# Optimization experiments

Measured on AMD Instinct MI355X. Metric: run time of the kernel, lower is better.

The kernel has to match this reference:

```python
import jax, jax.numpy as jnp
import numpy as np

ALG = 8  # octonion algebra dimension
_TRIPLES = [(1,2,3),(1,4,5),(1,7,6),(2,4,6),(2,5,7),(3,4,7),(3,6,5)]

def _oct_table():
    # Cayley multiplication table: e_i * e_j = S[i,j] * e_{K[i,j]}
    K = np.zeros((8,8), np.int64); S = np.zeros((8,8), np.int64)
    K[0,:] = np.arange(8); S[0,:] = 1
    K[:,0] = np.arange(8); S[:,0] = 1
    for i in range(1,8):
        K[i,i] = 0; S[i,i] = -1
    for (a,b,c) in _TRIPLES:
        for x,y,z in ((a,b,c),(b,c,a),(c,a,b)):
            K[x,y] = z; S[x,y] = 1
            K[y,x] = z; S[y,x] = -1
    return K, S

_K, _S = _oct_table()

def _ternary(w):
    # BitNet-style absmean ternary quantization (STE is irrelevant for fwd)
    scale = jnp.mean(jnp.abs(w)) + 1e-8
    wq = jnp.clip(jnp.round(w / scale), -1.0, 1.0) * scale
    return w + jax.lax.stop_gradient(wq - w)

def _oct_big(w):
    # w: [8, din8, dout8] -> structured dense [8*din8, 8*dout8]
    # out_k = sum_{i,j: e_i e_j = s e_k} s * x_i @ W_j  (64 static blocks)
    din8, dout8 = w.shape[1], w.shape[2]
    big = jnp.zeros((8, din8, 8, dout8), w.dtype)
    for i in range(8):
        for j in range(8):
            big = big.at[i, :, int(_K[i, j]), :].set(float(_S[i, j]) * w[j])
    return big.reshape(8 * din8, 8 * dout8)

def _oct_linear(x, w):
    return x @ _oct_big(_ternary(w))

def setup_inputs() -> dict:
    key = jax.random.key(0)
    k1, k2, k3, k4 = jax.random.split(key, 4)
    B, T, D = 8, 4096, 768
    H = 2048  # int(2*4*768/3) rounded up to multiple of 8
    d8, h8 = D // ALG, H // ALG
    x = jax.random.normal(k1, (B, T, D), dtype=jnp.float32)
    w_gate = 0.02 * jax.random.normal(k2, (ALG, d8, h8), dtype=jnp.float32)
    w_up   = 0.02 * jax.random.normal(k3, (ALG, d8, h8), dtype=jnp.float32)
    w_down = 0.02 * jax.random.normal(k4, (ALG, h8, d8), dtype=jnp.float32)
    return {"x": x, "w_gate": w_gate, "w_up": w_up, "w_down": w_down}

def reference(x, w_gate, w_up, w_down):
    gate = _oct_linear(x, w_gate)          # [B,T,H]
    up   = _oct_linear(x, w_up)            # [B,T,H]
    h    = jax.nn.silu(gate) * up          # SwiGLU gate
    return _oct_linear(h, w_down)          # [B,T,D]
```

## Files before the change

### kernel.cpp

```cpp
#include <hip/hip_runtime.h>
#include <hip/hip_bf16.h>

typedef unsigned short u16;
typedef unsigned int u32;
typedef float f32x4 __attribute__((ext_vector_type(4)));
typedef __bf16 bf16x8 __attribute__((ext_vector_type(8)));

#define AS1 __attribute__((address_space(1)))
#define AS3 __attribute__((address_space(3)))

#define MTOT 32768
#define DK   768
#define HN   2048

__constant__ signed char J_TAB[64] = {
  0,1,2,3,4,5,6,7,
  1,0,3,2,5,4,7,6,
  2,3,0,1,6,7,4,5,
  3,2,1,0,7,6,5,4,
  4,5,6,7,0,1,2,3,
  5,4,7,6,1,0,3,2,
  6,7,4,5,2,3,0,1,
  7,6,5,4,3,2,1,0};
__constant__ signed char S_TAB[64] = {
   1, 1, 1, 1, 1, 1, 1, 1,
  -1, 1,-1, 1,-1, 1, 1,-1,
  -1, 1, 1,-1,-1,-1, 1, 1,
  -1,-1, 1, 1,-1, 1,-1, 1,
  -1, 1, 1, 1, 1,-1,-1,-1,
  -1,-1, 1,-1, 1, 1, 1,-1,
  -1,-1,-1, 1, 1,-1, 1, 1,
  -1, 1,-1,-1, 1, 1,-1, 1};

__device__ __forceinline__ u16 f2bf(float f) {
  u32 x = __float_as_uint(f);
  x += 0x7fffu + ((x >> 16) & 1u);
  return (u16)(x >> 16);
}

__device__ __forceinline__ void gload_lds16(const void* g, void* l) {
  __builtin_amdgcn_global_load_lds((AS1 void*)(g), (AS3 void*)(l), 16, 0, 0);
}

#define VMW(N) do { __builtin_amdgcn_sched_barrier(0); \
  asm volatile("s_waitcnt vmcnt(" #N ")" ::: "memory"); \
  __builtin_amdgcn_sched_barrier(0); } while (0)
#define BAR() do { __builtin_amdgcn_sched_barrier(0); \
  __builtin_amdgcn_s_barrier(); \
  __builtin_amdgcn_sched_barrier(0); } while (0)

template <int LDK>
__device__ __forceinline__ void stage_half(const u16* __restrict__ src,
                                           u16* lds, int tid) {
#pragma unroll
  for (int f0 = 0; f0 < 1024; f0 += 512) {
    int flat = f0 + tid;
    int row = flat >> 3;
    int c = (flat & 7) ^ (row & 7);
    gload_lds16(src + row * LDK + c * 8, lds + (f0 + (tid & ~63)) * 8);
  }
}

template <int LDK, bool SA, bool SB, int VM>
__device__ __forceinline__ void ktile4(
    const u16* lAp, const u16* lBp, u16* lAn, u16* lBn,
    const u16* __restrict__ aStage, const u16* __restrict__ bStage,
    int tid, int arow, int brow, int c0, int c1, f32x4 (&acc)[8][4]) {
  bf16x8 a0[4], a1[4], a2[4], a3[4], b0[4], b1[4];
#pragma unroll
  for (int mi = 0; mi < 4; ++mi)
    a0[mi] = *(const bf16x8*)(lAp + (arow + mi * 16) * 64 + c0);
#pragma unroll
  for (int ni = 0; ni < 4; ++ni)
    b0[ni] = *(const bf16x8*)(lBp + (brow + ni * 16) * 64 + c0);
#pragma unroll
  for (int mi = 0; mi < 4; ++mi)
    a1[mi] = *(const bf16x8*)(lAp + (arow + mi * 16) * 64 + c1);
#pragma unroll
  for (int ni = 0; ni < 4; ++ni)
    b1[ni] = *(const bf16x8*)(lBp + (brow + ni * 16) * 64 + c1);
  if constexpr (SA) stage_half<LDK>(aStage, lAn, tid);
  BAR();
  __builtin_amdgcn_s_setprio(1);
#pragma unroll
  for (int mi = 0; mi < 4; ++mi)
#pragma unroll
    for (int ni = 0; ni < 4; ++ni)
      acc[mi][ni] = __builtin_amdgcn_mfma_f32_16x16x32_bf16(
          a0[mi], b0[ni], acc[mi][ni], 0, 0, 0);
  __builtin_amdgcn_s_setprio(0);
  BAR();
#pragma unroll
  for (int mi = 0; mi < 4; ++mi)
    a2[mi] = *(const bf16x8*)(lAp + (arow + 64 + mi * 16) * 64 + c0);
  if constexpr (SA) stage_half<LDK>(aStage + 128 * LDK, lAn + 128 * 64, tid);
  BAR();
  __builtin_amdgcn_s_setprio(1);
#pragma unroll
  for (int mi = 0; mi < 4; ++mi)
#pragma unroll
    for (int ni = 0; ni < 4; ++ni)
      acc[mi][ni] = __builtin_amdgcn_mfma_f32_16x16x32_bf16(
          a1[mi], b1[ni], acc[mi][ni], 0, 0, 0);
  __builtin_amdgcn_s_setprio(0);
  BAR();
#pragma unroll
  for (int mi = 0; mi < 4; ++mi)
    a3[mi] = *(const bf16x8*)(lAp + (arow + 64 + mi * 16) * 64 + c1);
  if constexpr (SB) stage_half<LDK>(bStage, lBn, tid);
  BAR();
  __builtin_amdgcn_s_setprio(1);
#pragma unroll
  for (int mi = 0; mi < 4; ++mi)
#pragma unroll
    for (int ni = 0; ni < 4; ++ni)
      acc[4 + mi][ni] = __builtin_amdgcn_mfma_f32_16x16x32_bf16(
          a2[mi], b0[ni], acc[4 + mi][ni], 0, 0, 0);
  __builtin_amdgcn_s_setprio(0);
  BAR();
  if constexpr (SB) stage_half<LDK>(bStage + 128 * LDK, lBn + 128 * 64, tid);
  if constexpr (VM == 4) VMW(4);
  else if constexpr (VM == 0) VMW(0);
  BAR();
  __builtin_amdgcn_s_setprio(1);
#pragma unroll
  for (int mi = 0; mi < 4; ++mi)
#pragma unroll
    for (int ni = 0; ni < 4; ++ni)
      acc[4 + mi][ni] = __builtin_amdgcn_mfma_f32_16x16x32_bf16(
          a3[mi], b1[ni], acc[4 + mi][ni], 0, 0, 0);
  __builtin_amdgcn_s_setprio(0);
  BAR();
}

template <int NK, int LDK>
__device__ __forceinline__ void gemm_core(const u16* __restrict__ aSrc,
                                          const u16* __restrict__ bSrc, int tid,
                                          u16* lA0, u16* lA1, u16* lB0, u16* lB1,
                                          f32x4 (&acc)[8][4]) {
  const int lane = tid & 63;
  const int wave = tid >> 6;
  const int wm = wave >> 2, wn = wave & 3;
  const int l15 = lane & 15, quad = (lane >> 4) & 3;
  const int arow = wm * 128 + l15;
  const int brow = wn * 64 + l15;
  const int c0 = (quad ^ (l15 & 7)) * 8;
  const int c1 = ((quad + 4) ^ (l15 & 7)) * 8;

  stage_half<LDK>(aSrc, lA0, tid);
  stage_half<LDK>(aSrc + 128 * LDK, lA0 + 128 * 64, tid);
  stage_half<LDK>(bSrc, lB0, tid);
  stage_half<LDK>(bSrc + 128 * LDK, lB0 + 128 * 64, tid);
  stage_half<LDK>(bSrc + 64, lB1, tid);
  stage_half<LDK>(bSrc + 64 + 128 * LDK, lB1 + 128 * 64, tid);
  VMW(4);
  BAR();

#pragma unroll 1
  for (int i = 0; i < NK / 2 - 1; ++i) {
    ktile4<LDK, true, true, 4>(lA0, lB0, lA1, lB0,
                               aSrc + (2 * i + 1) * 64, bSrc + (2 * i + 2) * 64,
                               tid, arow, brow, c0, c1, acc);
    ktile4<LDK, true, true, 4>(lA1, lB1, lA0, lB1,
                               aSrc + (2 * i + 2) * 64, bSrc + (2 * i + 3) * 64,
                               tid, arow, brow, c0, c1, acc);
  }
  ktile4<LDK, true, false, 0>(lA0, lB0, lA1, lB0,
                              aSrc + (NK - 1) * 64, nullptr,
                              tid, arow, brow, c0, c1, acc);
  ktile4<LDK, false, false, -1>(lA1, lB1, lA0, lB1, nullptr, nullptr,
                                tid, arow, brow, c0, c1, acc);
}

template <bool ST, int VM>
__device__ __forceinline__ void ktile2(
    const u16* lAp, const u16* lBp, u16* lAs, u16* lBs,
    const u16* __restrict__ aS, const u16* __restrict__ bS,
    int tid, int arow, int brow, int c0, int c1, f32x4 (&acc)[4][4]) {
  bf16x8 a0[4], a1[4], b0[4], b1[4];
#pragma unroll
  for (int mi = 0; mi < 4; ++mi)
    a0[mi] = *(const bf16x8*)(lAp + (arow + mi * 16) * 64 + c0);
#pragma unroll
  for (int ni = 0; ni < 4; ++ni)
    b0[ni] = *(const bf16x8*)(lBp + (brow + ni * 16) * 64 + c0);
#pragma unroll
  for (int mi = 0; mi < 4; ++mi)
    a1[mi] = *(const bf16x8*)(lAp + (arow + mi * 16) * 64 + c1);
#pragma unroll
  for (int ni = 0; ni < 4; ++ni)
    b1[ni] = *(const bf16x8*)(lBp + (brow + ni * 16) * 64 + c1);
  if constexpr (ST) stage_half<HN>(aS, lAs, tid);
  BAR();
  __builtin_amdgcn_s_setprio(1);
#pragma unroll
  for (int mi = 0; mi < 4; ++mi)
#pragma unroll
    for (int ni = 0; ni < 4; ++ni)
      acc[mi][ni] = __builtin_amdgcn_mfma_f32_16x16x32_bf16(
          a0[mi], b0[ni], acc[mi][ni], 0, 0, 0);
  __builtin_amdgcn_s_setprio(0);
  BAR();
  if constexpr (ST) {
    stage_half<HN>(bS, lBs, tid);
    stage_half<HN>(bS + 128 * HN, lBs + 128 * 64, tid);
  }
  if constexpr (VM == 6) VMW(6);
  else if constexpr (VM == 0) VMW(0);
  BAR();
  __builtin_amdgcn_s_setprio(1);
#pragma unroll
  for (int mi = 0; mi < 4; ++mi)
#pragma unroll
    for (int ni = 0; ni < 4; ++ni)
      acc[mi][ni] = __builtin_amdgcn_mfma_f32_16x16x32_bf16(
          a1[mi], b1[ni], acc[mi][ni], 0, 0, 0);
  __builtin_amdgcn_s_setprio(0);
  BAR();
}

__global__ void scales1_kernel(const float* __restrict__ w0,
                               const float* __restrict__ w1,
                               const float* __restrict__ w2,
                               float* __restrict__ partials) {
  __shared__ float red[256];
  const int t = blockIdx.x / 192;
  const int chunk = blockIdx.x % 192;
  const float* w = (t == 0) ? w0 : (t == 1) ? w1 : w2;
  const float4* w4 = (const float4*)(w + chunk * 1024);
  float4 v = w4[threadIdx.x];
  red[threadIdx.x] = fabsf(v.x) + fabsf(v.y) + fabsf(v.z) + fabsf(v.w);
  __syncthreads();
  for (int off = 128; off; off >>= 1) {
    if (threadIdx.x < off) red[threadIdx.x] += red[threadIdx.x + off];
    __syncthreads();
  }
  if (threadIdx.x == 0) partials[blockIdx.x] = red[0];
}

__global__ void scales2_kernel(const float* __restrict__ partials,
                               float* __restrict__ scales) {
  __shared__ float red[256];
  float s = (threadIdx.x < 192) ? partials[blockIdx.x * 192 + threadIdx.x] : 0.f;
  red[threadIdx.x] = s;
  __syncthreads();
  for (int off = 128; off; off >>= 1) {
    if (threadIdx.x < off) red[threadIdx.x] += red[threadIdx.x + off];
    __syncthreads();
  }
  if (threadIdx.x == 0) scales[blockIdx.x] = red[0] / 196608.f + 1e-8f;
}

__global__ void build_big_kernel(const float* __restrict__ w,
                                 const float* __restrict__ scales, int sidx,
                                 int A, int B, int ilv, u16* __restrict__ dst) {
  int idx = blockIdx.x * 256 + threadIdx.x;
  int K8 = 8 * A;
  int n = idx / K8;
  int k = idx - n * K8;
  int i = k / A, a = k - i * A;
  int c = n / B, b = n - c * B;
  float scale = scales[sidx];
  int j = J_TAB[i * 8 + c];
  float q = rintf(w[(j * A + a) * B + b] / scale);
  q = fminf(1.f, fmaxf(-1.f, q));
  int nd = (ilv >= 0) ? (((n & ~15) << 1) | (ilv << 4) | (n & 15)) : n;
  int kd = (ilv == -2) ? ((k & ~31) | ((k & 15) << 1) | ((k >> 4) & 1)) : k;
  dst[nd * K8 + kd] = f2bf(q * (float)S_TAB[i * 8 + c]);
}

__global__ void cvt_x_kernel(const float* __restrict__ x, u16* __restrict__ xb) {
  int gid = blockIdx.x * 256 + threadIdx.x;
  const float4* x4 = (const float4*)x;
  float4 v0 = x4[gid * 2], v1 = x4[gid * 2 + 1];
  uint4 o;
  o.x = (u32)f2bf(v0.x) | ((u32)f2bf(v0.y) << 16);
  o.y = (u32)f2bf(v0.z) | ((u32)f2bf(v0.w) << 16);
  o.z = (u32)f2bf(v1.x) | ((u32)f2bf(v1.y) << 16);
  o.w = (u32)f2bf(v1.z) | ((u32)f2bf(v1.w) << 16);
  ((uint4*)xb)[gid] = o;
}

__global__ __launch_bounds__(512, 2) void gemm1_kernel(
    const u16* __restrict__ xb, const u16* __restrict__ wgu,
    const float* __restrict__ scales, u16* __restrict__ h) {
  __shared__ __align__(16) u16 lA0[256 * 64], lA1[256 * 64];
  __shared__ __align__(16) u16 lB0[256 * 64], lB1[256 * 64];
  const int tid = threadIdx.x;
  const int logical = (blockIdx.x & 7) * 256 + (blockIdx.x >> 3);
  const int bn = logical & 15;
  const int bm = logical >> 4;
  const int m0 = bm * 256, n0 = bn * 256;

  f32x4 acc[8][4] = {};
  gemm_core<12, DK>(xb + (size_t)m0 * DK, wgu + (size_t)n0 * DK, tid,
                    lA0, lA1, lB0, lB1, acc);

  const int lane = tid & 63, wave = tid >> 6;
  const int wm = wave >> 2, wn = wave & 3;
  const int l15 = lane & 15, quad = lane >> 4;
  const float sg = scales[0], su = scales[1];
  const int a_ = bn * 4 + wn;
  u32* h32 = (u32*)h;
#pragma unroll
  for (int mi = 0; mi < 8; ++mi)
#pragma unroll
    for (int r = 0; r < 4; ++r) {
      int m = m0 + wm * 128 + mi * 16 + quad * 4 + r;
      float g0 = acc[mi][0][r] * sg, u0 = acc[mi][1][r] * su;
      float g1 = acc[mi][2][r] * sg, u1 = acc[mi][3][r] * su;
      float h0 = g0 / (1.f + __expf(-g0)) * u0;
      float h1 = g1 / (1.f + __expf(-g1)) * u1;
      h32[(size_t)m * (HN / 2) + a_ * 16 + l15] =
          (u32)f2bf(h0) | ((u32)f2bf(h1) << 16);
    }
}

__global__ __launch_bounds__(512, 2) void gemm2_kernel(
    const u16* __restrict__ h, const u16* __restrict__ wd,
    const float* __restrict__ scales, float* __restrict__ out) {
  __shared__ __align__(16) u16 lA[3][128 * 64];
  __shared__ __align__(16) u16 lB[3][256 * 64];
  const int tid = threadIdx.x;
  const int logical = (blockIdx.x & 7) * 96 + (blockIdx.x >> 3);
  const int bn = logical % 3;
  const int bm = logical / 3;
  const int m0 = bm * 128, n0 = bn * 256;
  const u16* aSrc = h + (size_t)m0 * HN;
  const u16* bSrc = wd + (size_t)n0 * HN;

  const int lane = tid & 63, wave = tid >> 6;
  const int wm = wave >> 2, wn = wave & 3;
  const int l15 = lane & 15, quad = (lane >> 4) & 3;
  const int arow = wm * 64 + l15;
  const int brow = wn * 64 + l15;
  const int c0 = (quad ^ (l15 & 7)) * 8;
  const int c1 = ((quad + 4) ^ (l15 & 7)) * 8;

  f32x4 acc[4][4] = {};

  stage_half<HN>(aSrc, lA[0], tid);
  stage_half<HN>(bSrc, lB[0], tid);
  stage_half<HN>(bSrc + 128 * HN, lB[0] + 128 * 64, tid);
  stage_half<HN>(aSrc + 64, lA[1], tid);
  stage_half<HN>(bSrc + 64, lB[1], tid);
  stage_half<HN>(bSrc + 64 + 128 * HN, lB[1] + 128 * 64, tid);
  VMW(6);
  BAR();

  u16 *pA0 = lA[0], *pA1 = lA[1], *pA2 = lA[2];
  u16 *pB0 = lB[0], *pB1 = lB[1], *pB2 = lB[2];
#pragma unroll 1
  for (int S = 0; S < (HN / 64) - 2; ++S) {
    ktile2<true, 6>(pA0, pB0, pA2, pB2,
                    aSrc + (S + 2) * 64, bSrc + (S + 2) * 64,
                    tid, arow, brow, c0, c1, acc);
    u16* tA = pA0; pA0 = pA1; pA1 = pA2; pA2 = tA;
    u16* tB = pB0; pB0 = pB1; pB1 = pB2; pB2 = tB;
  }
  ktile2<false, 0>(pA0, pB0, nullptr, nullptr, nullptr, nullptr,
                   tid, arow, brow, c0, c1, acc);
  ktile2<false, -1>(pA1, pB1, nullptr, nullptr, nullptr, nullptr,
                    tid, arow, brow, c0, c1, acc);

  const float sd = scales[2];
#pragma unroll
  for (int mi = 0; mi < 4; ++mi)
#pragma unroll
    for (int ni = 0; ni < 4; ++ni) {
      const int n = n0 + wn * 64 + ni * 16 + l15;
#pragma unroll
      for (int r = 0; r < 4; ++r) {
        int m = m0 + wm * 64 + mi * 16 + quad * 4 + r;
        out[(size_t)m * DK + n] = acc[mi][ni][r] * sd;
      }
    }
}

extern "C" void kernel_launch(void* const* d_in, const int* in_sizes, int n_in,
                              void* d_out, int out_size, void* d_ws, size_t ws_size,
                              hipStream_t stream) {
  const float* x      = (const float*)d_in[0];
  const float* w_gate = (const float*)d_in[1];
  const float* w_up   = (const float*)d_in[2];
  const float* w_down = (const float*)d_in[3];
  float* out = (float*)d_out;

  char* ws = (char*)d_ws;
  float* scales   = (float*)ws;
  float* partials = (float*)(ws + 256);
  u16* wgu = (u16*)(ws + 4096);
  u16* wd  = (u16*)(ws + 4096 + 6291456u);
  u16* xb  = (u16*)(ws + 4096 + 9437184u);
  u16* h   = (u16*)(ws + 4096 + 9437184u + 50331648u);

  scales1_kernel<<<576, 256, 0, stream>>>(w_gate, w_up, w_down, partials);
  scales2_kernel<<<3, 256, 0, stream>>>(partials, scales);
  build_big_kernel<<<6144, 256, 0, stream>>>(w_gate, scales, 0, 96, 256, 0, wgu);
  build_big_kernel<<<6144, 256, 0, stream>>>(w_up,   scales, 1, 96, 256, 1, wgu);
  build_big_kernel<<<6144, 256, 0, stream>>>(w_down, scales, 2, 256, 96, -2, wd);
  cvt_x_kernel<<<12288, 256, 0, stream>>>(x, xb);
  gemm1_kernel<<<2048, 512, 0, stream>>>(xb, wgu, scales, h);
  gemm2_kernel<<<768, 512, 0, stream>>>(h, wd, scales, out);
}
```

Before: 552.1 us.

## Shrink gemm2 tile to 64x256 with 4 waves and double buffering

Rewrites the down-projection GEMM to use 256-thread blocks, each computing a 64x256 output tile, with a simple two-stage LDS double buffer in place of the three-stage split-half pipeline. The launch grows to 1536 blocks, which gives more blocks per CU and spreads work more evenly across the device. The cost is lower arithmetic intensity per block: the 256-row B tile is reloaded for half as many A rows, raising global and LDS traffic. The simpler schedule also does less to overlap loads with MFMA work.

```diff
diff --git a/kernel.cpp b/kernel.cpp
--- a/kernel.cpp
+++ b/kernel.cpp
@@ -61,6 +61,18 @@
   }
 }
 
+template <int ROWS, int LDK>
+__device__ __forceinline__ void stage_tile(const u16* __restrict__ src,
+                                           u16* lds, int tid) {
+#pragma unroll
+  for (int f0 = 0; f0 < ROWS * 8; f0 += 256) {
+    int flat = f0 + tid;
+    int row = flat >> 3;
+    int c = (flat & 7) ^ (row & 7);
+    gload_lds16(src + row * LDK + c * 8, lds + (f0 + (tid & 192)) * 8);
+  }
+}
+
 template <int LDK, bool SA, bool SB, int VM>
 __device__ __forceinline__ void ktile4(
     const u16* lAp, const u16* lBp, u16* lAn, u16* lBn,
@@ -170,53 +182,6 @@
                               tid, arow, brow, c0, c1, acc);
   ktile4<LDK, false, false, -1>(lA1, lB1, lA0, lB1, nullptr, nullptr,
                                 tid, arow, brow, c0, c1, acc);
-}
-
-template <bool ST, int VM>
-__device__ __forceinline__ void ktile2(
-    const u16* lAp, const u16* lBp, u16* lAs, u16* lBs,
-    const u16* __restrict__ aS, const u16* __restrict__ bS,
-    int tid, int arow, int brow, int c0, int c1, f32x4 (&acc)[4][4]) {
-  bf16x8 a0[4], a1[4], b0[4], b1[4];
-#pragma unroll
-  for (int mi = 0; mi < 4; ++mi)
-    a0[mi] = *(const bf16x8*)(lAp + (arow + mi * 16) * 64 + c0);
-#pragma unroll
-  for (int ni = 0; ni < 4; ++ni)
-    b0[ni] = *(const bf16x8*)(lBp + (brow + ni * 16) * 64 + c0);
-#pragma unroll
-  for (int mi = 0; mi < 4; ++mi)
-    a1[mi] = *(const bf16x8*)(lAp + (arow + mi * 16) * 64 + c1);
-#pragma unroll
-  for (int ni = 0; ni < 4; ++ni)
-    b1[ni] = *(const bf16x8*)(lBp + (brow + ni * 16) * 64 + c1);
-  if constexpr (ST) stage_half<HN>(aS, lAs, tid);
-  BAR();
-  __builtin_amdgcn_s_setprio(1);
-#pragma unroll
-  for (int mi = 0; mi < 4; ++mi)
-#pragma unroll
-    for (int ni = 0; ni < 4; ++ni)
-      acc[mi][ni] = __builtin_amdgcn_mfma_f32_16x16x32_bf16(
-          a0[mi], b0[ni], acc[mi][ni], 0, 0, 0);
-  __builtin_amdgcn_s_setprio(0);
-  BAR();
-  if constexpr (ST) {
-    stage_half<HN>(bS, lBs, tid);
-    stage_half<HN>(bS + 128 * HN, lBs + 128 * 64, tid);
-  }
-  if constexpr (VM == 6) VMW(6);
-  else if constexpr (VM == 0) VMW(0);
-  BAR();
-  __builtin_amdgcn_s_setprio(1);
-#pragma unroll
-  for (int mi = 0; mi < 4; ++mi)
-#pragma unroll
-    for (int ni = 0; ni < 4; ++ni)
-      acc[mi][ni] = __builtin_amdgcn_mfma_f32_16x16x32_bf16(
-          a1[mi], b1[ni], acc[mi][ni], 0, 0, 0);
-  __builtin_amdgcn_s_setprio(0);
-  BAR();
 }
 
 __global__ void scales1_kernel(const float* __restrict__ w0,
@@ -316,62 +281,77 @@
     }
 }
 
-__global__ __launch_bounds__(512, 2) void gemm2_kernel(
+__global__ __launch_bounds__(256, 2) void gemm2_kernel(
     const u16* __restrict__ h, const u16* __restrict__ wd,
     const float* __restrict__ scales, float* __restrict__ out) {
-  __shared__ __align__(16) u16 lA[3][128 * 64];
-  __shared__ __align__(16) u16 lB[3][256 * 64];
+  __shared__ __align__(16) u16 lA[2][64 * 64];
+  __shared__ __align__(16) u16 lB[2][256 * 64];
   const int tid = threadIdx.x;
-  const int logical = (blockIdx.x & 7) * 96 + (blockIdx.x >> 3);
+  const int logical = (blockIdx.x & 7) * 192 + (blockIdx.x >> 3);
   const int bn = logical % 3;
   const int bm = logical / 3;
-  const int m0 = bm * 128, n0 = bn * 256;
+  const int m0 = bm * 64, n0 = bn * 256;
   const u16* aSrc = h + (size_t)m0 * HN;
   const u16* bSrc = wd + (size_t)n0 * HN;
 
   const int lane = tid & 63, wave = tid >> 6;
-  const int wm = wave >> 2, wn = wave & 3;
   const int l15 = lane & 15, quad = (lane >> 4) & 3;
-  const int arow = wm * 64 + l15;
-  const int brow = wn * 64 + l15;
+  const int brow = wave * 64 + l15;
   const int c0 = (quad ^ (l15 & 7)) * 8;
   const int c1 = ((quad + 4) ^ (l15 & 7)) * 8;
 
   f32x4 acc[4][4] = {};
 
-  stage_half<HN>(aSrc, lA[0], tid);
-  stage_half<HN>(bSrc, lB[0], tid);
-  stage_half<HN>(bSrc + 128 * HN, lB[0] + 128 * 64, tid);
-  stage_half<HN>(aSrc + 64, lA[1], tid);
-  stage_half<HN>(bSrc + 64, lB[1], tid);
-  stage_half<HN>(bSrc + 64 + 128 * HN, lB[1] + 128 * 64, tid);
-  VMW(6);
-  BAR();
-
-  u16 *pA0 = lA[0], *pA1 = lA[1], *pA2 = lA[2];
-  u16 *pB0 = lB[0], *pB1 = lB[1], *pB2 = lB[2];
+  stage_tile<64, HN>(aSrc, lA[0], tid);
+  stage_tile<256, HN>(bSrc, lB[0], tid);
+
 #pragma unroll 1
-  for (int S = 0; S < (HN / 64) - 2; ++S) {
-    ktile2<true, 6>(pA0, pB0, pA2, pB2,
-                    aSrc + (S + 2) * 64, bSrc + (S + 2) * 64,
-                    tid, arow, brow, c0, c1, acc);
-    u16* tA = pA0; pA0 = pA1; pA1 = pA2; pA2 = tA;
-    u16* tB = pB0; pB0 = pB1; pB1 = pB2; pB2 = tB;
-  }
-  ktile2<false, 0>(pA0, pB0, nullptr, nullptr, nullptr, nullptr,
-                   tid, arow, brow, c0, c1, acc);
-  ktile2<false, -1>(pA1, pB1, nullptr, nullptr, nullptr, nullptr,
-                    tid, arow, brow, c0, c1, acc);
+  for (int S = 0; S < HN / 64; ++S) {
+    if (S < HN / 64 - 1) {
+      stage_tile<64, HN>(aSrc + (S + 1) * 64, lA[(S + 1) & 1], tid);
+      stage_tile<256, HN>(bSrc + (S + 1) * 64, lB[(S + 1) & 1], tid);
+      VMW(10);
+    } else {
+      VMW(0);
+    }
+    BAR();
+    const u16* la = lA[S & 1];
+    const u16* lb = lB[S & 1];
+    bf16x8 af[4][2], bf[4][2];
+#pragma unroll
+    for (int mi = 0; mi < 4; ++mi) {
+      const u16* p = la + (l15 + mi * 16) * 64;
+      af[mi][0] = *(const bf16x8*)(p + c0);
+      af[mi][1] = *(const bf16x8*)(p + c1);
+    }
+#pragma unroll
+    for (int ni = 0; ni < 4; ++ni) {
+      const u16* p = lb + (brow + ni * 16) * 64;
+      bf[ni][0] = *(const bf16x8*)(p + c0);
+      bf[ni][1] = *(const bf16x8*)(p + c1);
+    }
+    __builtin_amdgcn_s_setprio(1);
+#pragma unroll
+    for (int k = 0; k < 2; ++k)
+#pragma unroll
+      for (int mi = 0; mi < 4; ++mi)
+#pragma unroll
+        for (int ni = 0; ni < 4; ++ni)
+          acc[mi][ni] = __builtin_amdgcn_mfma_f32_16x16x32_bf16(
+              af[mi][k], bf[ni][k], acc[mi][ni], 0, 0, 0);
+    __builtin_amdgcn_s_setprio(0);
+    BAR();
+  }
 
   const float sd = scales[2];
 #pragma unroll
   for (int mi = 0; mi < 4; ++mi)
 #pragma unroll
     for (int ni = 0; ni < 4; ++ni) {
-      const int n = n0 + wn * 64 + ni * 16 + l15;
+      const int n = n0 + wave * 64 + ni * 16 + l15;
 #pragma unroll
       for (int r = 0; r < 4; ++r) {
-        int m = m0 + wm * 64 + mi * 16 + quad * 4 + r;
+        int m = m0 + mi * 16 + quad * 4 + r;
         out[(size_t)m * DK + n] = acc[mi][ni][r] * sd;
       }
     }
@@ -401,5 +381,5 @@
   build_big_kernel<<<6144, 256, 0, stream>>>(w_down, scales, 2, 256, 96, -2, wd);
   cvt_x_kernel<<<12288, 256, 0, stream>>>(x, xb);
   gemm1_kernel<<<2048, 512, 0, stream>>>(xb, wgu, scales, h);
-  gemm2_kernel<<<768, 512, 0, stream>>>(h, wd, scales, out);
-}
+  gemm2_kernel<<<1536, 256, 0, stream>>>(h, wd, scales, out);
+}
```

Result: slower. 572.2 us (+3.7%).
